# Performance work log

Measured on AMD Instinct MI355X. Metric: run time of the kernel, lower is better.

## Reference

```python
import jax, jax.numpy as jnp
import numpy as np
import math

B, N, D, H = 32, 512, 512, 8  # batch, num_neurons(=seq len=input_size), d_model, n_head
DH = D // H


def setup_inputs() -> dict:
    key = jax.random.key(0)
    ks = jax.random.split(key, 20)
    g = lambda k, shape, fan_in: jax.random.normal(k, shape, dtype=jnp.float32) / np.sqrt(fan_in)
    return {
        "x": jax.random.normal(ks[0], (B, N), dtype=jnp.float32),
        # per-neuron Linear(1, d_model): weight [N, D], bias [N, D]
        "W_emb": g(ks[1], (N, D), 1),
        "b_emb": g(ks[2], (N, D), 1),
        # MHA projections (stored [in, out])
        "Wq": g(ks[3], (D, D), D), "bq": jnp.zeros((D,), jnp.float32),
        "Wk": g(ks[4], (D, D), D), "bk": jnp.zeros((D,), jnp.float32),
        "Wv": g(ks[5], (D, D), D), "bv": jnp.zeros((D,), jnp.float32),
        "Wo": g(ks[6], (D, D), D), "bo": jnp.zeros((D,), jnp.float32),
        # per-neuron Linear(d_model, 1): weight [N, D], bias [N]
        "W_un": g(ks[7], (N, D), D),
        "b_un": jnp.zeros((N,), jnp.float32),
        # ff1: 512 -> 2048 -> 512 -> 256 (no activations)
        "W1": g(ks[8], (N, 2048), N), "b1": jnp.zeros((2048,), jnp.float32),
        "W2": g(ks[9], (2048, 512), 2048), "b2": jnp.zeros((512,), jnp.float32),
        "W3": g(ks[10], (512, 256), 512), "b3": jnp.zeros((256,), jnp.float32),
    }


def _forward(x, W_emb, b_emb, Wq, bq, Wk, bk, Wv, bv, Wo, bo, W_un, b_un, W1, b1, W2, b2, W3, b3):
    # Embedding: batched rank-1 'linear' per neuron -> [B, N, D]
    h = x[:, :, None] * W_emb[None] + b_emb[None]
    # MHA (note: positional encoding in the original is computed but unused)
    q = (h @ Wq + bq).reshape(B, N, H, DH).transpose(0, 2, 1, 3)
    k = (h @ Wk + bk).reshape(B, N, H, DH).transpose(0, 2, 1, 3)
    v = (h @ Wv + bv).reshape(B, N, H, DH).transpose(0, 2, 1, 3)
    scores = jnp.einsum('bhnd,bhmd->bhnm', q, k) / math.sqrt(DH)
    attn = jax.nn.softmax(scores, axis=-1)
    o = jnp.einsum('bhnm,bhmd->bhnd', attn, v)
    o = o.transpose(0, 2, 1, 3).reshape(B, N, D)
    o = o @ Wo + bo  # [B, N, D]
    # unEmbedding: per-neuron Linear(D, 1) -> [B, N, 1]
    x_atten = (jnp.einsum('bnd,nd->bn', o, W_un) + b_un)[:, :, None]
    # ff1 on squeezed [B, N]
    y = x_atten[..., 0]
    y = ((y @ W1 + b1) @ W2 + b2) @ W3 + b3  # [B, 256]
    y = y.reshape(-1, 1, 8, 32)
    # bilinear upsample to (16, 64), half-pixel centers (torch align_corners=False)
    y = jax.image.resize(y, (y.shape[0], 1, 16, 64), method='bilinear')
    y_min = y.min(axis=(2, 3), keepdims=True)
    y_max = y.max(axis=(2, 3), keepdims=True)
    y = (y - y_min) / (y_max - y_min + 1e-8)
    return y, x_atten


def reference(x, W_emb, b_emb, Wq, bq, Wk, bk, Wv, bv, Wo, bo, W_un, b_un, W1, b1, W2, b2, W3, b3):
    y, x_atten = _forward(x, W_emb, b_emb, Wq, bq, Wk, bk, Wv, bv, Wo, bo, W_un, b_un, W1, b1, W2, b2, W3, b3)
    # return_attn=False path: attention_weights is None (omitted)
    return (y, x_atten)
```

## Files before the change

### kernel.cpp

```cpp
#include <hip/hip_runtime.h>

#define B_  32
#define N_  512
#define D_  512
#define H_  8
#define DH_ 64
#define M_  (B_*N_)

typedef __attribute__((ext_vector_type(4))) float          f32x4;
typedef __attribute__((ext_vector_type(4))) unsigned short us4;
typedef __attribute__((ext_vector_type(8))) unsigned short us8;
typedef __attribute__((ext_vector_type(8))) __bf16         bf16x8;

__device__ __forceinline__ f32x4 mfma_bf16(us8 a, us8 b, f32x4 c) {
  return __builtin_amdgcn_mfma_f32_16x16x32_bf16(
      __builtin_bit_cast(bf16x8, a), __builtin_bit_cast(bf16x8, b), c, 0, 0, 0);
}

__device__ __forceinline__ unsigned short f2bf(float f) {
  return __builtin_bit_cast(unsigned short, (__bf16)f);
}

__device__ __forceinline__ float bf2f(unsigned short u) {
  return __builtin_bit_cast(float, (unsigned)u << 16);
}

__device__ __forceinline__ float fexp2(float x) {
  float r;
  asm("v_exp_f32 %0, %1" : "=v"(r) : "v"(x));
  return r;
}

__device__ __forceinline__ us8 ldg8(const unsigned short* p) {
  return *reinterpret_cast<const us8*>(p);
}

typedef const unsigned int __attribute__((address_space(1)))* gas_ptr;
typedef unsigned int __attribute__((address_space(3)))* las_ptr;

__device__ __forceinline__ void gload16(const unsigned short* src, unsigned short* ldsdst) {
  __builtin_amdgcn_global_load_lds((gas_ptr)(const void*)src, (las_ptr)(void*)ldsdst, 16, 0, 0);
}

__global__ __launch_bounds__(256) void k_pre(
    const float* __restrict__ W_emb, const float* __restrict__ b_emb,
    const float* __restrict__ Wun, const float* __restrict__ Wo,
    const float* __restrict__ Wq, const float* __restrict__ Wk,
    const float* __restrict__ Wv,
    const float* __restrict__ W1, const float* __restrict__ W2,
    const float* __restrict__ W3,
    const float* __restrict__ bo, const float* __restrict__ bun,
    unsigned short* __restrict__ P0, unsigned short* __restrict__ WunBf,
    unsigned short* __restrict__ WoBf, unsigned short* __restrict__ wT,
    unsigned short* __restrict__ w1T, unsigned short* __restrict__ w2T,
    unsigned short* __restrict__ w3T, float* __restrict__ cb,
    float* __restrict__ xa) {
  __shared__ float t[32][33];
  int id = blockIdx.x, tid = threadIdx.x;

  if (id < 1024) {
    int idx = id * 256 + tid;
    const float* src; unsigned short* dst; int off;
    if (idx < 65536)        { src = W_emb; dst = P0;          off = idx; }
    else if (idx < 131072)  { src = b_emb; dst = P0 + 262144; off = idx - 65536; }
    else if (idx < 196608)  { src = Wun;   dst = WunBf;       off = idx - 131072; }
    else                    { src = Wo;    dst = WoBf;        off = idx - 196608; }
    f32x4 v = *reinterpret_cast<const f32x4*>(src + (size_t)off * 4);
    us4 o;
#pragma unroll
    for (int e = 0; e < 4; ++e) o[e] = f2bf(v[e]);
    *reinterpret_cast<us4*>(dst + (size_t)off * 4) = o;
    return;
  }

  if (id >= 4096) {
    int idx = (id - 4096) * 256 + tid;
    *reinterpret_cast<f32x4*>(xa + (size_t)idx * 4) = (f32x4){0.f, 0.f, 0.f, 0.f};
    return;
  }

  if (id >= 3968) {
    int n = (id - 3968) * 4 + (tid >> 6);
    int lane = tid & 63;
    const float* a = Wun + (size_t)n * 512 + lane * 8;
    const float* b = bo + lane * 8;
    f32x4 a0 = *reinterpret_cast<const f32x4*>(a);
    f32x4 a1 = *reinterpret_cast<const f32x4*>(a + 4);
    f32x4 b0 = *reinterpret_cast<const f32x4*>(b);
    f32x4 b1 = *reinterpret_cast<const f32x4*>(b + 4);
    float s = a0[0]*b0[0] + a0[1]*b0[1] + a0[2]*b0[2] + a0[3]*b0[3]
            + a1[0]*b1[0] + a1[1]*b1[1] + a1[2]*b1[2] + a1[3]*b1[3];
#pragma unroll
    for (int off = 32; off; off >>= 1) s += __shfl_xor(s, off, 64);
    if (lane == 0) cb[n] = s + bun[n];
    return;
  }

  const float* src; unsigned short* dst; int R, C, bx, by;
  if (id < 1792) {
    int t3 = id - 1024, z = t3 >> 8, rem = t3 & 255;
    src = (z == 0) ? Wq : (z == 1) ? Wk : Wv;
    dst = wT + (size_t)z * (512 * 512);
    R = 512; C = 512; bx = rem & 15; by = rem >> 4;
  } else if (id < 2816) {
    int tr = id - 1792;
    src = W1; dst = w1T; R = 512; C = 2048; bx = tr & 63; by = tr >> 6;
  } else if (id < 3840) {
    int tr = id - 2816;
    src = W2; dst = w2T; R = 2048; C = 512; bx = tr & 15; by = tr >> 4;
  } else {
    int tr = id - 3840;
    src = W3; dst = w3T; R = 512; C = 256; bx = tr & 7; by = tr >> 3;
  }
  int c0 = bx * 32, r0 = by * 32;
  int tx = tid & 31, ty = tid >> 5;
  for (int yy = ty; yy < 32; yy += 8)
    t[yy][tx] = src[(size_t)(r0 + yy) * C + c0 + tx];
  __syncthreads();
  for (int yy = ty; yy < 32; yy += 8)
    dst[(size_t)(c0 + yy) * R + r0 + tx] = f2bf(t[tx][yy]);
}

__global__ __launch_bounds__(256, 4) void k_prep(
    const unsigned short* __restrict__ P0,
    const unsigned short* __restrict__ wT,
    const unsigned short* __restrict__ WunBf,
    const unsigned short* __restrict__ WoBf,
    const float* __restrict__ bq, const float* __restrict__ bk,
    const float* __restrict__ bv,
    unsigned short* __restrict__ P1,
    unsigned short* __restrict__ vpre,
    unsigned short* __restrict__ wEff) {
  __shared__ __align__(16) unsigned short lds[2][2 * 64 * 64];
  const int K = 512;
  int nwg = gridDim.x;
  int cpx = nwg >> 3;
  int wgid = ((int)blockIdx.x & 7) * cpx + ((int)blockIdx.x >> 3);
  bool p1 = wgid < 384;
  int lid = p1 ? wgid : wgid - 384;
  int ntiles = p1 ? 24 : 8;
  const unsigned short* A  = p1 ? P0 : WunBf;
  const unsigned short* Bt = p1 ? wT : WoBf;
  int mt = lid / ntiles, nt = lid - mt * ntiles;
  int m0 = mt * 64, n0 = nt * 64;
  int tid = threadIdx.x, wave = tid >> 6, lane = tid & 63;
  int lrow = lane & 15, g = lane >> 4;

  f32x4 acc[4];
#pragma unroll
  for (int i = 0; i < 4; ++i) acc[i] = (f32x4){0.f, 0.f, 0.f, 0.f};

  int rseg_base = wave * 8 + (lane >> 3);
  int coff = (((lane & 7) ^ (lane >> 3)) << 3);

#pragma unroll
  for (int i = 0; i < 2; ++i) {
    int rs = i * 32 + rseg_base;
    gload16(A  + (size_t)(m0 + rs) * K + coff, &lds[0][(i * 4 + wave) * 512]);
    gload16(Bt + (size_t)(n0 + rs) * K + coff, &lds[0][4096 + (i * 4 + wave) * 512]);
  }
  __syncthreads();

  for (int ks = 0; ks < 8; ++ks) {
    if (ks < 7) {
      int k0 = (ks + 1) * 64;
      int buf = (ks + 1) & 1;
#pragma unroll
      for (int i = 0; i < 2; ++i) {
        int rs = i * 32 + rseg_base;
        gload16(A  + (size_t)(m0 + rs) * K + k0 + coff, &lds[buf][(i * 4 + wave) * 512]);
        gload16(Bt + (size_t)(n0 + rs) * K + k0 + coff, &lds[buf][4096 + (i * 4 + wave) * 512]);
      }
    }
    const char* la = (const char*)&lds[ks & 1][0];
    const char* lb = la + 8192;
    int sw = (lrow & 7) << 4;
#pragma unroll
    for (int kk = 0; kk < 2; ++kk) {
      us8 aF = *reinterpret_cast<const us8*>(
          la + (wave * 16 + lrow) * 128 + ((kk * 64 + g * 16) ^ sw));
      us8 bF[4];
#pragma unroll
      for (int ni = 0; ni < 4; ++ni)
        bF[ni] = *reinterpret_cast<const us8*>(
            lb + (ni * 16 + lrow) * 128 + ((kk * 64 + g * 16) ^ sw));
#pragma unroll
      for (int ni = 0; ni < 4; ++ni)
        acc[ni] = mfma_bf16(aF, bF[ni], acc[ni]);
    }
    __syncthreads();
  }

  if (p1) {
#pragma unroll
    for (int ni = 0; ni < 4; ++ni) {
      int j = n0 + ni * 16 + lrow;
      int which = j >> 9, jj = j & 511;
      float bj = (which == 0 ? bq : which == 1 ? bk : bv)[jj];
#pragma unroll
      for (int r = 0; r < 4; ++r) {
        int mrow = m0 + wave * 16 + g * 4 + r;
        int isB = mrow >> 9, n = mrow & 511;
        unsigned short v16 = f2bf(acc[ni][r] + (isB ? bj : 0.f));
        if (which < 2) P1[(size_t)mrow * 1536 + j] = v16;
        else           vpre[(size_t)isB * 262144 + (size_t)jj * 512 + n] = v16;
      }
    }
  } else {
#pragma unroll
    for (int ni = 0; ni < 4; ++ni) {
      int j = n0 + ni * 16 + lrow;
#pragma unroll
      for (int r = 0; r < 4; ++r) {
        int mrow = m0 + wave * 16 + g * 4 + r;
        wEff[(size_t)mrow * 512 + j] = f2bf(acc[ni][r]);
      }
    }
  }
}

__global__ __launch_bounds__(512, 4) void k_attn(
    const float* __restrict__ x,
    const unsigned short* __restrict__ P1,
    const unsigned short* __restrict__ vpre,
    const unsigned short* __restrict__ wEff,
    float* __restrict__ xa) {
  __shared__ __align__(16) unsigned short kbuf[4096];
  __shared__ __align__(16) unsigned short vbuf[4096];
  __shared__ __align__(16) unsigned short pbuf[8][1024];
  int L = blockIdx.x;
  int chunk = (L >> 3) & 1;
  int bh = ((L & 7) << 5) | (L >> 4);
  int b = bh >> 3, h = bh & 7;
  int w = threadIdx.x >> 6, lane = threadIdx.x & 63;
  int lr = lane & 15, g = lane >> 4;
  const float cexp = 0.18033688011112042f;
  const float* xb = x + b * 512;

  us8 bq[2][2];
#pragma unroll
  for (int tt = 0; tt < 2; ++tt) {
    int n = chunk * 256 + w * 32 + tt * 16 + lr;
    float xv = xb[n];
#pragma unroll
    for (int hh = 0; hh < 2; ++hh) {
      int col = h * 64 + hh * 32 + g * 8;
      us8 a = ldg8(P1 + (size_t)n * 1536 + col);
      us8 bb = ldg8(P1 + (size_t)(512 + n) * 1536 + col);
      us8 o8;
#pragma unroll
      for (int e = 0; e < 8; ++e) o8[e] = f2bf(cexp * (xv * bf2f(a[e]) + bf2f(bb[e])));
      bq[tt][hh] = o8;
    }
  }

  f32x4 oacc[2][4];
#pragma unroll
  for (int tt = 0; tt < 2; ++tt)
#pragma unroll
    for (int db = 0; db < 4; ++db) oacc[tt][db] = (f32x4){0.f, 0.f, 0.f, 0.f};
  float lrun[2] = {0.f, 0.f};

  int kcol = 512 + h * 64 + (w & 1) * 32 + g * 8;
  int vdh  = h * 64 + (w >> 1) * 16 + lr;
  const unsigned short* vp0 = vpre + (size_t)vdh * 512;
  const unsigned short* vp1 = vp0 + 262144;
  char* pw = (char*)&pbuf[w][0];

  for (int mb = 0; mb < 8; ++mb) {
    if (mb > 0) __syncthreads();

    {
      int nK = mb * 64 + (w >> 1) * 16 + lr;
      float xk = xb[nK];
      us8 a = ldg8(P1 + (size_t)nK * 1536 + kcol);
      us8 bb = ldg8(P1 + (size_t)(512 + nK) * 1536 + kcol);
      us8 o8;
#pragma unroll
      for (int e = 0; e < 8; ++e) o8[e] = f2bf(xk * bf2f(a[e]) + bf2f(bb[e]));
      *reinterpret_cast<us8*>((char*)kbuf + w * 1024 + lane * 16) = o8;
    }
    {
      int n0 = mb * 64 + (w & 1) * 32 + g * 8;
      us8 a = ldg8(vp0 + n0);
      us8 bb = ldg8(vp1 + n0);
      f32x4 x0 = *reinterpret_cast<const f32x4*>(xb + n0);
      f32x4 x1 = *reinterpret_cast<const f32x4*>(xb + n0 + 4);
      us8 o8;
#pragma unroll
      for (int e = 0; e < 8; ++e) {
        float xe = (e < 4) ? x0[e] : x1[e - 4];
        o8[e] = f2bf(xe * bf2f(a[e]) + bf2f(bb[e]));
      }
      *reinterpret_cast<us8*>((char*)vbuf + w * 1024 + lane * 16) = o8;
    }
    __syncthreads();

    const char* kb = (const char*)kbuf;
    const char* vb = (const char*)vbuf;

#pragma unroll
    for (int tt = 0; tt < 2; ++tt) {
      f32x4 s[4];
      __builtin_amdgcn_s_setprio(1);
#pragma unroll
      for (int mc_l = 0; mc_l < 4; ++mc_l) {
        f32x4 a = (f32x4){0.f, 0.f, 0.f, 0.f};
        a = mfma_bf16(*(const us8*)(kb + (mc_l * 2 + 0) * 1024 + lane * 16), bq[tt][0], a);
        a = mfma_bf16(*(const us8*)(kb + (mc_l * 2 + 1) * 1024 + lane * 16), bq[tt][1], a);
        s[mc_l] = a;
      }
      __builtin_amdgcn_s_setprio(0);
      float lsum = 0.f;
#pragma unroll
      for (int mc_l = 0; mc_l < 4; ++mc_l) {
#pragma unroll
        for (int r = 0; r < 4; ++r) {
          float p = fexp2(s[mc_l][r]);
          s[mc_l][r] = p;
          lsum += p;
        }
      }
      lrun[tt] += lsum;
#pragma unroll
      for (int mc_l = 0; mc_l < 4; ++mc_l) {
        uint2 u;
        u.x = (unsigned)f2bf(s[mc_l][0]) | ((unsigned)f2bf(s[mc_l][1]) << 16);
        u.y = (unsigned)f2bf(s[mc_l][2]) | ((unsigned)f2bf(s[mc_l][3]) << 16);
        unsigned off = (unsigned)((mc_l >> 1) * 1024 + (((mc_l & 1) << 1) | (g >> 1)) * 256
                                  + lr * 16 + (g & 1) * 8);
        *reinterpret_cast<uint2*>(pw + off) = u;
      }
      __builtin_amdgcn_s_setprio(1);
#pragma unroll
      for (int ks = 0; ks < 2; ++ks) {
        us8 bp = *(const us8*)(pw + ks * 1024 + lane * 16);
#pragma unroll
        for (int db = 0; db < 4; ++db) {
          us8 av = *(const us8*)(vb + (db * 2 + ks) * 1024 + lane * 16);
          oacc[tt][db] = mfma_bf16(av, bp, oacc[tt][db]);
        }
      }
      __builtin_amdgcn_s_setprio(0);
    }
  }

#pragma unroll
  for (int tt = 0; tt < 2; ++tt) {
    float tot = lrun[tt];
    tot += __shfl_xor(tot, 16, 64);
    tot += __shfl_xor(tot, 32, 64);
    float inv = 1.f / tot;
    int nmod = chunk * 256 + w * 32 + tt * 16 + lr;
    const unsigned short* wrow = wEff + (size_t)nmod * 512 + h * 64 + g * 4;
    float part = 0.f;
#pragma unroll
    for (int db = 0; db < 4; ++db) {
      us4 wv = *reinterpret_cast<const us4*>(wrow + db * 16);
#pragma unroll
      for (int r = 0; r < 4; ++r) part += oacc[tt][db][r] * bf2f(wv[r]);
    }
    part *= inv;
    part += __shfl_xor(part, 16, 64);
    part += __shfl_xor(part, 32, 64);
    if (g == 0) atomicAdd(&xa[b * 512 + nmod], part);
  }
}

__global__ __launch_bounds__(256) void k_xafin(
    const float* __restrict__ xa, const float* __restrict__ cb,
    float* __restrict__ out_xa, unsigned short* __restrict__ xabf) {
  int m = blockIdx.x * 256 + threadIdx.x;
  float v = xa[m] + cb[m & (N_ - 1)];
  out_xa[m] = v;
  xabf[m] = f2bf(v);
}

__global__ __launch_bounds__(256) void k_ffmm(
    const unsigned short* __restrict__ A,
    const unsigned short* __restrict__ Bt,
    const float* __restrict__ bias, int K, int N,
    unsigned short* __restrict__ obf) {
  int wave = threadIdx.x >> 6, lane = threadIdx.x & 63;
  int lrow = lane & 15, g = lane >> 4;
  int j = blockIdx.x * 64 + wave * 16 + lrow;
  f32x4 acc0 = (f32x4){0.f, 0.f, 0.f, 0.f}, acc1 = acc0;
  const unsigned short* brow = Bt + (size_t)j * K;
  for (int k0 = g * 8; k0 < K; k0 += 32) {
    us8 bfr = ldg8(brow + k0);
    acc0 = mfma_bf16(ldg8(A + (size_t)lrow * K + k0), bfr, acc0);
    acc1 = mfma_bf16(ldg8(A + (size_t)(16 + lrow) * K + k0), bfr, acc1);
  }
  float bj = bias[j];
#pragma unroll
  for (int r = 0; r < 4; ++r) {
    int mA = g * 4 + r, mB = 16 + g * 4 + r;
    obf[(size_t)mA * N + j] = f2bf(acc0[r] + bj);
    obf[(size_t)mB * N + j] = f2bf(acc1[r] + bj);
  }
}

__global__ __launch_bounds__(256) void k_ffmm2(
    const unsigned short* __restrict__ A,
    const unsigned short* __restrict__ Bt,
    float* __restrict__ y2p) {
  int ks = blockIdx.x >> 3, nb = blockIdx.x & 7;
  int wave = threadIdx.x >> 6, lane = threadIdx.x & 63;
  int lrow = lane & 15, g = lane >> 4;
  int j = nb * 64 + wave * 16 + lrow;
  const int K = 2048;
  f32x4 acc0 = (f32x4){0.f, 0.f, 0.f, 0.f}, acc1 = acc0;
  const unsigned short* brow = Bt + (size_t)j * K;
#pragma unroll
  for (int i = 0; i < 8; ++i) {
    int k0 = ks * 256 + i * 32 + g * 8;
    us8 bfr = ldg8(brow + k0);
    acc0 = mfma_bf16(ldg8(A + (size_t)lrow * K + k0), bfr, acc0);
    acc1 = mfma_bf16(ldg8(A + (size_t)(16 + lrow) * K + k0), bfr, acc1);
  }
  float* out = y2p + (size_t)ks * 16384;
#pragma unroll
  for (int r = 0; r < 4; ++r) {
    out[(size_t)(g * 4 + r) * 512 + j] = acc0[r];
    out[(size_t)(16 + g * 4 + r) * 512 + j] = acc1[r];
  }
}

__global__ __launch_bounds__(256) void k_ff3up(
    const float* __restrict__ y2p,
    const unsigned short* __restrict__ w3T,
    const float* __restrict__ b2, const float* __restrict__ b3,
    float* __restrict__ out) {
  __shared__ float y2l[512];
  __shared__ float y3[256];
  __shared__ float red[8];
  int b = blockIdx.x, t = threadIdx.x;
#pragma unroll
  for (int hh = 0; hh < 2; ++hh) {
    int d = t + hh * 256;
    float v = b2[d];
#pragma unroll
    for (int s = 0; s < 8; ++s) v += y2p[(size_t)s * 16384 + (size_t)b * 512 + d];
    y2l[d] = v;
  }
  __syncthreads();
  const unsigned short* wrow = w3T + (size_t)t * 512;
  float s = b3[t];
  for (int d8 = 0; d8 < 64; ++d8) {
    us8 wv = ldg8(wrow + d8 * 8);
#pragma unroll
    for (int e = 0; e < 8; ++e) s += y2l[d8 * 8 + e] * bf2f(wv[e]);
  }
  y3[t] = s;
  __syncthreads();
  float vals[4];
  float mn = 3.0e38f, mx = -3.0e38f;
#pragma unroll
  for (int p2 = 0; p2 < 4; ++p2) {
    int p = t * 4 + p2;
    int i = p >> 6, jj = p & 63;
    float sy = fmaxf((float)i * 0.5f - 0.25f, 0.0f);
    int y0 = (int)sy; float fy = sy - (float)y0;
    int y1i = min(y0 + 1, 7);
    float sx = fmaxf((float)jj * 0.5f - 0.25f, 0.0f);
    int x0 = (int)sx; float fx = sx - (float)x0;
    int x1 = min(x0 + 1, 31);
    float v00 = y3[y0 * 32 + x0], v01 = y3[y0 * 32 + x1];
    float v10 = y3[y1i * 32 + x0], v11 = y3[y1i * 32 + x1];
    float v = (1.f - fy) * ((1.f - fx) * v00 + fx * v01)
            +        fy  * ((1.f - fx) * v10 + fx * v11);
    vals[p2] = v;
    mn = fminf(mn, v); mx = fmaxf(mx, v);
  }
#pragma unroll
  for (int off = 32; off; off >>= 1) {
    mn = fminf(mn, __shfl_xor(mn, off, 64));
    mx = fmaxf(mx, __shfl_xor(mx, off, 64));
  }
  int wv2 = t >> 6;
  if ((t & 63) == 0) { red[wv2] = mn; red[4 + wv2] = mx; }
  __syncthreads();
  mn = fminf(fminf(red[0], red[1]), fminf(red[2], red[3]));
  mx = fmaxf(fmaxf(red[4], red[5]), fmaxf(red[6], red[7]));
  float inv = 1.f / (mx - mn + 1e-8f);
#pragma unroll
  for (int p2 = 0; p2 < 4; ++p2)
    out[(size_t)b * 1024 + t * 4 + p2] = (vals[p2] - mn) * inv;
}

extern "C" void kernel_launch(void* const* d_in, const int* in_sizes, int n_in,
                              void* d_out, int out_size, void* d_ws, size_t ws_size,
                              hipStream_t stream) {
  const float* x     = (const float*)d_in[0];
  const float* W_emb = (const float*)d_in[1];
  const float* b_emb = (const float*)d_in[2];
  const float* Wq    = (const float*)d_in[3];
  const float* bq    = (const float*)d_in[4];
  const float* Wk    = (const float*)d_in[5];
  const float* bk    = (const float*)d_in[6];
  const float* Wv    = (const float*)d_in[7];
  const float* bv    = (const float*)d_in[8];
  const float* Wo    = (const float*)d_in[9];
  const float* bo    = (const float*)d_in[10];
  const float* W_un  = (const float*)d_in[11];
  const float* b_un  = (const float*)d_in[12];
  const float* W1    = (const float*)d_in[13];
  const float* b1    = (const float*)d_in[14];
  const float* W2    = (const float*)d_in[15];
  const float* b2    = (const float*)d_in[16];
  const float* W3    = (const float*)d_in[17];
  const float* b3    = (const float*)d_in[18];

  char* ws = (char*)d_ws;
  unsigned short* P0    = (unsigned short*)(ws + 0);
  unsigned short* P1    = (unsigned short*)(ws + 1048576);
  unsigned short* vpre  = (unsigned short*)(ws + 4194304);
  unsigned short* WunBf = (unsigned short*)(ws + 5242880);
  unsigned short* WoBf  = (unsigned short*)(ws + 5767168);
  unsigned short* wT    = (unsigned short*)(ws + 67108864);
  unsigned short* wEff  = (unsigned short*)(ws + 68681728);
  float*          cb    = (float*)(ws + 69206016);
  unsigned short* xabf  = (unsigned short*)(ws + 69208064);
  float*          xa    = (float*)(ws + 69240832);
  unsigned short* w1T   = (unsigned short*)(ws + 83886080);
  unsigned short* w2T   = (unsigned short*)(ws + 85983232);
  unsigned short* w3T   = (unsigned short*)(ws + 88080384);
  unsigned short* y1bf  = (unsigned short*)(ws + 88342528);
  float*          y2p   = (float*)(ws + 94371840);

  float* out_y  = (float*)d_out;
  float* out_xa = ((float*)d_out) + 32768;

  k_pre<<<dim3(4112), dim3(256), 0, stream>>>(
      W_emb, b_emb, W_un, Wo, Wq, Wk, Wv, W1, W2, W3, bo, b_un,
      P0, WunBf, WoBf, wT, w1T, w2T, w3T, cb, xa);

  k_prep<<<dim3(448), dim3(256), 0, stream>>>(
      P0, wT, WunBf, WoBf, bq, bk, bv, P1, vpre, wEff);

  k_attn<<<dim3(512), dim3(512), 0, stream>>>(x, P1, vpre, wEff, xa);

  k_xafin<<<dim3(64), dim3(256), 0, stream>>>(xa, cb, out_xa, xabf);

  k_ffmm<<<dim3(32), dim3(256), 0, stream>>>(xabf, w1T, b1, 512, 2048, y1bf);
  k_ffmm2<<<dim3(64), dim3(256), 0, stream>>>(y1bf, w2T, y2p);

  k_ff3up<<<dim3(B_), dim3(256), 0, stream>>>(y2p, w3T, b2, b3, out_y);
}
```

Before: 80.16 us.

## Split attention key range across two blocks and combine partial softmax sums

Each (batch, head, query-half) tile now also splits the key range in half, which doubles the attention grid to 1024 blocks. Unnormalised partial outputs and partial softmax denominators go to per-head buffers through atomics, and the final xa kernel does the division and sums over heads. The goal is better CU occupancy and load balance for the attention stage. In exchange it adds a larger zeroing pass, more atomics and a heavier finalisation step. The launch-bounds occupancy hint is also raised, which may tighten register limits and cause spills.

Result: slower. 173.0 us (+115.8%).

```diff
diff --git a/kernel.cpp b/kernel.cpp
--- a/kernel.cpp
+++ b/kernel.cpp
@@ -54,7 +54,7 @@
     unsigned short* __restrict__ WoBf, unsigned short* __restrict__ wT,
     unsigned short* __restrict__ w1T, unsigned short* __restrict__ w2T,
     unsigned short* __restrict__ w3T, float* __restrict__ cb,
-    float* __restrict__ xa) {
+    float* __restrict__ zbase) {
   __shared__ float t[32][33];
   int id = blockIdx.x, tid = threadIdx.x;
 
@@ -75,7 +75,7 @@
 
   if (id >= 4096) {
     int idx = (id - 4096) * 256 + tid;
-    *reinterpret_cast<f32x4*>(xa + (size_t)idx * 4) = (f32x4){0.f, 0.f, 0.f, 0.f};
+    *reinterpret_cast<f32x4*>(zbase + (size_t)idx * 4) = (f32x4){0.f, 0.f, 0.f, 0.f};
     return;
   }
 
@@ -219,18 +219,19 @@
   }
 }
 
-__global__ __launch_bounds__(512, 4) void k_attn(
+__global__ __launch_bounds__(512, 8) void k_attn(
     const float* __restrict__ x,
     const unsigned short* __restrict__ P1,
     const unsigned short* __restrict__ vpre,
     const unsigned short* __restrict__ wEff,
-    float* __restrict__ xa) {
+    float* __restrict__ xp, float* __restrict__ ls2) {
   __shared__ __align__(16) unsigned short kbuf[4096];
   __shared__ __align__(16) unsigned short vbuf[4096];
   __shared__ __align__(16) unsigned short pbuf[8][1024];
   int L = blockIdx.x;
-  int chunk = (L >> 3) & 1;
-  int bh = ((L & 7) << 5) | (L >> 4);
+  int bh = ((L & 7) << 5) | (L >> 5);
+  int sub = (L >> 3) & 3;
+  int nhalf = sub & 1, mhalf = sub >> 1;
   int b = bh >> 3, h = bh & 7;
   int w = threadIdx.x >> 6, lane = threadIdx.x & 63;
   int lr = lane & 15, g = lane >> 4;
@@ -240,7 +241,7 @@
   us8 bq[2][2];
 #pragma unroll
   for (int tt = 0; tt < 2; ++tt) {
-    int n = chunk * 256 + w * 32 + tt * 16 + lr;
+    int n = nhalf * 256 + w * 32 + tt * 16 + lr;
     float xv = xb[n];
 #pragma unroll
     for (int hh = 0; hh < 2; ++hh) {
@@ -266,12 +267,13 @@
   const unsigned short* vp0 = vpre + (size_t)vdh * 512;
   const unsigned short* vp1 = vp0 + 262144;
   char* pw = (char*)&pbuf[w][0];
-
-  for (int mb = 0; mb < 8; ++mb) {
+  int mbase = mhalf * 256;
+
+  for (int mb = 0; mb < 4; ++mb) {
     if (mb > 0) __syncthreads();
 
     {
-      int nK = mb * 64 + (w >> 1) * 16 + lr;
+      int nK = mbase + mb * 64 + (w >> 1) * 16 + lr;
       float xk = xb[nK];
       us8 a = ldg8(P1 + (size_t)nK * 1536 + kcol);
       us8 bb = ldg8(P1 + (size_t)(512 + nK) * 1536 + kcol);
@@ -281,7 +283,7 @@
       *reinterpret_cast<us8*>((char*)kbuf + w * 1024 + lane * 16) = o8;
     }
     {
-      int n0 = mb * 64 + (w & 1) * 32 + g * 8;
+      int n0 = mbase + mb * 64 + (w & 1) * 32 + g * 8;
       us8 a = ldg8(vp0 + n0);
       us8 bb = ldg8(vp1 + n0);
       f32x4 x0 = *reinterpret_cast<const f32x4*>(xb + n0);
@@ -350,8 +352,7 @@
     float tot = lrun[tt];
     tot += __shfl_xor(tot, 16, 64);
     tot += __shfl_xor(tot, 32, 64);
-    float inv = 1.f / tot;
-    int nmod = chunk * 256 + w * 32 + tt * 16 + lr;
+    int nmod = nhalf * 256 + w * 32 + tt * 16 + lr;
     const unsigned short* wrow = wEff + (size_t)nmod * 512 + h * 64 + g * 4;
     float part = 0.f;
 #pragma unroll
@@ -360,18 +361,28 @@
 #pragma unroll
       for (int r = 0; r < 4; ++r) part += oacc[tt][db][r] * bf2f(wv[r]);
     }
-    part *= inv;
     part += __shfl_xor(part, 16, 64);
     part += __shfl_xor(part, 32, 64);
-    if (g == 0) atomicAdd(&xa[b * 512 + nmod], part);
+    if (g == 0) {
+      atomicAdd(&xp[(size_t)bh * 512 + nmod], part);
+      atomicAdd(&ls2[(size_t)bh * 512 + nmod], tot);
+    }
   }
 }
 
 __global__ __launch_bounds__(256) void k_xafin(
-    const float* __restrict__ xa, const float* __restrict__ cb,
+    const float* __restrict__ xp, const float* __restrict__ ls2,
+    const float* __restrict__ cb,
     float* __restrict__ out_xa, unsigned short* __restrict__ xabf) {
   int m = blockIdx.x * 256 + threadIdx.x;
-  float v = xa[m] + cb[m & (N_ - 1)];
+  int b = m >> 9, n = m & 511;
+  float v = 0.f;
+#pragma unroll
+  for (int h = 0; h < 8; ++h) {
+    size_t i = ((size_t)(b * 8 + h) << 9) | n;
+    v += xp[i] / ls2[i];
+  }
+  v += cb[n];
   out_xa[m] = v;
   xabf[m] = f2bf(v);
 }
@@ -521,7 +532,8 @@
   unsigned short* wEff  = (unsigned short*)(ws + 68681728);
   float*          cb    = (float*)(ws + 69206016);
   unsigned short* xabf  = (unsigned short*)(ws + 69208064);
-  float*          xa    = (float*)(ws + 69240832);
+  float*          xp    = (float*)(ws + 69240832);
+  float*          ls2   = (float*)(ws + 69765120);
   unsigned short* w1T   = (unsigned short*)(ws + 83886080);
   unsigned short* w2T   = (unsigned short*)(ws + 85983232);
   unsigned short* w3T   = (unsigned short*)(ws + 88080384);
@@ -531,16 +543,16 @@
   float* out_y  = (float*)d_out;
   float* out_xa = ((float*)d_out) + 32768;
 
-  k_pre<<<dim3(4112), dim3(256), 0, stream>>>(
+  k_pre<<<dim3(4352), dim3(256), 0, stream>>>(
       W_emb, b_emb, W_un, Wo, Wq, Wk, Wv, W1, W2, W3, bo, b_un,
-      P0, WunBf, WoBf, wT, w1T, w2T, w3T, cb, xa);
+      P0, WunBf, WoBf, wT, w1T, w2T, w3T, cb, xp);
 
   k_prep<<<dim3(448), dim3(256), 0, stream>>>(
       P0, wT, WunBf, WoBf, bq, bk, bv, P1, vpre, wEff);
 
-  k_attn<<<dim3(512), dim3(512), 0, stream>>>(x, P1, vpre, wEff, xa);
-
-  k_xafin<<<dim3(64), dim3(256), 0, stream>>>(xa, cb, out_xa, xabf);
+  k_attn<<<dim3(1024), dim3(512), 0, stream>>>(x, P1, vpre, wEff, xp, ls2);
+
+  k_xafin<<<dim3(64), dim3(256), 0, stream>>>(xp, ls2, cb, out_xa, xabf);
 
   k_ffmm<<<dim3(32), dim3(256), 0, stream>>>(xabf, w1T, b1, 512, 2048, y1bf);
   k_ffmm2<<<dim3(64), dim3(256), 0, stream>>>(y1bf, w2T, y2p);
```
